# Optimization experiments

Measured on AMD Instinct MI355X. Metric: run time of the kernel, lower is better.

Reference implementation:

```python
import jax, jax.numpy as jnp
import numpy as np

B, T, F_DIM = 256, 96, 368
D_MODEL = min(768, F_DIM)   # d_model = min(hidden_dim, feat_dim)
NUM_CLASSES = 29
WINDOW = 5


def setup_inputs() -> dict:
    key = jax.random.key(0)
    ks = jax.random.split(key, 12)
    s_in = 1.0 / np.sqrt(F_DIM)
    s_h = 1.0 / np.sqrt(D_MODEL)
    return {
        "features": jax.random.normal(ks[0], (B, T, F_DIM), jnp.float32),
        "hand": jax.random.uniform(ks[1], (B, 2), jnp.float32),
        # single-layer GRU params (torch layout: (3H, in) / (3H, H))
        "gru_Wi": jax.random.normal(ks[2], (3 * D_MODEL, F_DIM), jnp.float32) * s_in,
        "gru_Wh": jax.random.normal(ks[3], (3 * D_MODEL, D_MODEL), jnp.float32) * s_h,
        "gru_bi": jax.random.normal(ks[4], (3 * D_MODEL,), jnp.float32) * s_h,
        "gru_bh": jax.random.normal(ks[5], (3 * D_MODEL,), jnp.float32) * s_h,
        # coarse predictor: Linear(d_model, 2)
        "Wc": jax.random.normal(ks[6], (2, D_MODEL), jnp.float32) * s_h,
        "bc": jax.random.normal(ks[7], (2,), jnp.float32) * s_h,
        # fine predictor: Linear(d_model, num_classes)
        "Wf": jax.random.normal(ks[8], (NUM_CLASSES, D_MODEL), jnp.float32) * s_h,
        "bf": jax.random.normal(ks[9], (NUM_CLASSES,), jnp.float32) * s_h,
    }


def _gru(x, Wi, Wh, bi, bh):
    """Single-layer unidirectional GRU (torch gate math). x: (B,T,F) -> (B,T,H)."""
    H = Wh.shape[1]
    xproj = jnp.einsum("btf,gf->btg", x, Wi) + bi  # (B,T,3H)

    def step(h, xt):
        gi_r, gi_z, gi_n = jnp.split(xt, 3, axis=-1)
        gh = h @ Wh.T + bh
        gh_r, gh_z, gh_n = jnp.split(gh, 3, axis=-1)
        r = jax.nn.sigmoid(gi_r + gh_r)
        z = jax.nn.sigmoid(gi_z + gh_z)
        n = jnp.tanh(gi_n + r * gh_n)
        h_new = (1.0 - z) * n + z * h
        return h_new, h_new

    h0 = jnp.zeros((x.shape[0], H), x.dtype)
    _, hs = jax.lax.scan(step, h0, jnp.swapaxes(xproj, 0, 1))  # (T,B,H)
    return jnp.swapaxes(hs, 0, 1)


def _apply_nms(scores):
    """Vectorized version of the per-position sliding-window min suppression.
    scores: (B,T,2). Keep row i iff scores[:, i, 0] equals the min of its
    window of size WINDOW (clipped at sequence boundaries)."""
    bg = scores[..., 0]  # (B,T)
    half = WINDOW // 2
    padded = jnp.pad(bg, ((0, 0), (half, half)), constant_values=jnp.inf)
    Tlen = bg.shape[1]
    shifts = jnp.stack([padded[:, k:k + Tlen] for k in range(WINDOW)], axis=0)
    wmin = jnp.min(shifts, axis=0)  # (B,T)
    keep = (bg == wmin)[..., None]
    return jnp.where(keep, scores, jnp.zeros_like(scores))


def reference(features, hand, gru_Wi, gru_Wh, gru_bi, gru_bh, Wc, bc, Wf, bf):
    # hand is accepted (matching the torch forward signature) but unused there too.
    temporal = _gru(features, gru_Wi, gru_Wh, gru_bi, gru_bh)  # (B,T,D)
    coarse_logits = temporal @ Wc.T + bc                        # (B,T,2)
    fine_logits = temporal @ Wf.T + bf                          # (B,T,C)
    coarse_scores = jax.nn.softmax(coarse_logits, axis=2)
    fine_scores = jax.nn.sigmoid(fine_logits)
    coarse_nms = _apply_nms(coarse_scores)
    coarse_decisions = jnp.argmax(coarse_nms, axis=2)
    return coarse_decisions, coarse_nms, fine_scores
```

## Files before the change

kernel.cpp:

```cpp
#include <hip/hip_runtime.h>
#include <hip/hip_bf16.h>

#define B_ 256
#define T_ 96
#define F_ 368
#define H_ 368
#define G3_ 1104
#define NC_ 29
#define BT_ (B_*T_)
#define HB_ (H_*B_)

#define NSL 8
#define NU 46
#define NCOL 138
#define ROWS 8
#define WQCOLS 1152

#define WQ2_U16 (8*9*12*2*64*8)

#define F4C(v, i) ((i)==0?(v).x:((i)==1?(v).y:((i)==2?(v).z:(v).w)))

typedef __attribute__((ext_vector_type(8))) short bhalf8;
typedef __attribute__((ext_vector_type(4))) float f32x4;

__device__ __forceinline__ unsigned short f2bf(float x) {
    unsigned u = __float_as_uint(x);
    u += 0x7fffu + ((u >> 16) & 1u);
    return (unsigned short)(u >> 16);
}
__device__ __forceinline__ float bf2f(unsigned short b) {
    return __uint_as_float(((unsigned)b) << 16);
}

__device__ __forceinline__ void gll16(const void* g, void* l) {
    __builtin_amdgcn_global_load_lds(
        (const __attribute__((address_space(1))) void*)g,
        (__attribute__((address_space(3))) void*)l, 16, 0, 0);
}

__device__ __forceinline__ int bload_i(const int* p) {
    return __hip_atomic_load(p, __ATOMIC_RELAXED, __HIP_MEMORY_SCOPE_AGENT);
}
__device__ __forceinline__ void bstore_i(int* p, int v) {
    __hip_atomic_store(p, v, __ATOMIC_RELAXED, __HIP_MEMORY_SCOPE_AGENT);
}
__device__ __forceinline__ unsigned int bload_u(const unsigned int* p) {
    return __hip_atomic_load(p, __ATOMIC_RELAXED, __HIP_MEMORY_SCOPE_AGENT);
}
__device__ __forceinline__ void bstore_u(unsigned int* p, unsigned int v) {
    __hip_atomic_store(p, v, __ATOMIC_RELAXED, __HIP_MEMORY_SCOPE_AGENT);
}

__global__ __launch_bounds__(256) void k_prep_wq2(const float* __restrict__ Wh,
                                                  unsigned short* __restrict__ Wq2) {
    const int idx = blockIdx.x*256 + threadIdx.x;
    const int l = idx & 63;
    const int p = (idx >> 6) & 1;
    int q = idx >> 7;
    const int kt = q % 12; q /= 12;
    const int nt = q % 9;
    const int us = q / 9;
    const int col = nt*16 + (l & 15);
    const int k0 = kt*32 + (l >> 4)*8;
    float v[8];
    #pragma unroll
    for (int e = 0; e < 8; ++e) v[e] = 0.f;
    if (col < NCOL && k0 < H_) {
        const int g = col / NU, uu = col - g*NU;
        const int grow = g*H_ + us*NU + uu;
        const float4 f0 = *reinterpret_cast<const float4*>(Wh + (size_t)grow*H_ + k0);
        const float4 f1 = *reinterpret_cast<const float4*>(Wh + (size_t)grow*H_ + k0 + 4);
        v[0]=f0.x; v[1]=f0.y; v[2]=f0.z; v[3]=f0.w;
        v[4]=f1.x; v[5]=f1.y; v[6]=f1.z; v[7]=f1.w;
    }
    unsigned int o[4];
    #pragma unroll
    for (int e = 0; e < 4; ++e) {
        const unsigned short h0 = f2bf(v[2*e]), h1 = f2bf(v[2*e+1]);
        const unsigned short w0 = p ? f2bf(v[2*e]   - bf2f(h0)) : h0;
        const unsigned short w1 = p ? f2bf(v[2*e+1] - bf2f(h1)) : h1;
        o[e] = (unsigned)w0 | ((unsigned)w1 << 16);
    }
    uint4* dst = reinterpret_cast<uint4*>(Wq2 + (size_t)idx*8);
    *dst = make_uint4(o[0], o[1], o[2], o[3]);
}

__global__ __launch_bounds__(256) void k_prep_wcat(const float* __restrict__ Wc,
                                                   const float* __restrict__ Wf,
                                                   float* __restrict__ Wcat) {
    const int idx = blockIdx.x*256 + threadIdx.x;
    const int u = idx >> 5, c = idx & 31;
    float v = 0.f;
    if (c < 2) v = Wc[c*H_ + u];
    else if (c < 31) v = Wf[(c-2)*H_ + u];
    Wcat[idx] = v;
}

__global__ __launch_bounds__(256) void k_zero_bar(int* __restrict__ bar) {
    __hip_atomic_store(bar + blockIdx.x*256 + threadIdx.x, 0,
                       __ATOMIC_RELAXED, __HIP_MEMORY_SCOPE_AGENT);
}

__global__ __launch_bounds__(256) void k_split_a(const float* __restrict__ src,
                                                 unsigned short* __restrict__ Ah,
                                                 unsigned short* __restrict__ Al) {
    const int idx = blockIdx.x*256 + threadIdx.x;
    const float4 v = reinterpret_cast<const float4*>(src)[idx];
    ushort4 h, lo;
    h.x = f2bf(v.x); lo.x = f2bf(v.x - bf2f(h.x));
    h.y = f2bf(v.y); lo.y = f2bf(v.y - bf2f(h.y));
    h.z = f2bf(v.z); lo.z = f2bf(v.z - bf2f(h.z));
    h.w = f2bf(v.w); lo.w = f2bf(v.w - bf2f(h.w));
    reinterpret_cast<ushort4*>(Ah)[idx] = h;
    reinterpret_cast<ushort4*>(Al)[idx] = lo;
}

__global__ __launch_bounds__(256) void k_split_b(const float* __restrict__ Wi,
                                                 unsigned short* __restrict__ Bh,
                                                 unsigned short* __restrict__ Bl) {
    const int idx = blockIdx.x*256 + threadIdx.x;
    const float x = (idx < G3_*F_) ? Wi[idx] : 0.f;
    const unsigned short h = f2bf(x);
    Bh[idx] = h;
    Bl[idx] = f2bf(x - bf2f(h));
}

__global__ __launch_bounds__(256) void k_xproj_mfma(
        const unsigned short* __restrict__ Ah, const unsigned short* __restrict__ Al,
        const unsigned short* __restrict__ Bh, const unsigned short* __restrict__ Bl,
        const float* __restrict__ bias, float* __restrict__ C)
{
    __shared__ unsigned short sAh[128*32], sAl[128*32], sBh[128*32], sBl[128*32];
    const int tid = threadIdx.x;
    const int w   = tid >> 6, l = tid & 63;
    const int gm0 = blockIdx.y * 128, gn0 = blockIdx.x * 128;

    const int srow = tid >> 2;
    const int cg   = (tid & 3) ^ ((tid >> 3) & 3);
    const size_t aoff0 = (size_t)(gm0 + srow)      * F_ + cg * 8;
    const size_t aoff1 = (size_t)(gm0 + srow + 64) * F_ + cg * 8;
    const size_t boff0 = (size_t)(gn0 + srow)      * F_ + cg * 8;
    const size_t boff1 = (size_t)(gn0 + srow + 64) * F_ + cg * 8;
    const int lb0 = w * 1024, lb1 = 4096 + w * 1024;

    const int lr = l & 15, lk = l >> 4;
    const int cswz = (lk ^ ((lr >> 1) & 3)) * 16;
    const int wr = w >> 1, wc = w & 1;
    int offA[4], offB[4];
    #pragma unroll
    for (int f = 0; f < 4; ++f) {
        offA[f] = (wr*64 + f*16 + lr) * 64 + cswz;
        offB[f] = (wc*64 + f*16 + lr) * 64 + cswz;
    }

    f32x4 acc[4][4];
    #pragma unroll
    for (int i = 0; i < 4; ++i)
        #pragma unroll
        for (int j = 0; j < 4; ++j) acc[i][j] = f32x4{0.f,0.f,0.f,0.f};

    auto stage = [&](int kt) {
        const size_t ko = (size_t)kt * 32;
        gll16(Ah + aoff0 + ko, (char*)sAh + lb0);
        gll16(Ah + aoff1 + ko, (char*)sAh + lb1);
        gll16(Al + aoff0 + ko, (char*)sAl + lb0);
        gll16(Al + aoff1 + ko, (char*)sAl + lb1);
        gll16(Bh + boff0 + ko, (char*)sBh + lb0);
        gll16(Bh + boff1 + ko, (char*)sBh + lb1);
        gll16(Bl + boff0 + ko, (char*)sBl + lb0);
        gll16(Bl + boff1 + ko, (char*)sBl + lb1);
    };

    stage(0);
    for (int kt = 0; kt < 12; ++kt) {
        __syncthreads();
        if (kt == 11) {
            if (cg >= 2) {
                const f32x4 z = f32x4{0.f,0.f,0.f,0.f};
                *reinterpret_cast<f32x4*>((char*)sAh + tid*16)        = z;
                *reinterpret_cast<f32x4*>((char*)sAh + tid*16 + 4096) = z;
                *reinterpret_cast<f32x4*>((char*)sAl + tid*16)        = z;
                *reinterpret_cast<f32x4*>((char*)sAl + tid*16 + 4096) = z;
                *reinterpret_cast<f32x4*>((char*)sBh + tid*16)        = z;
                *reinterpret_cast<f32x4*>((char*)sBh + tid*16 + 4096) = z;
                *reinterpret_cast<f32x4*>((char*)sBl + tid*16)        = z;
                *reinterpret_cast<f32x4*>((char*)sBl + tid*16 + 4096) = z;
            }
            __syncthreads();
        }
        bhalf8 fAh[4], fAl[4], fBh[4], fBl[4];
        #pragma unroll
        for (int f = 0; f < 4; ++f) {
            fAh[f] = *reinterpret_cast<const bhalf8*>((const char*)sAh + offA[f]);
            fAl[f] = *reinterpret_cast<const bhalf8*>((const char*)sAl + offA[f]);
            fBh[f] = *reinterpret_cast<const bhalf8*>((const char*)sBh + offB[f]);
            fBl[f] = *reinterpret_cast<const bhalf8*>((const char*)sBl + offB[f]);
        }
        __syncthreads();
        if (kt < 11) stage(kt + 1);
        #pragma unroll
        for (int i = 0; i < 4; ++i)
            #pragma unroll
            for (int j = 0; j < 4; ++j) {
                acc[i][j] = __builtin_amdgcn_mfma_f32_16x16x32_bf16(fAh[i], fBh[j], acc[i][j], 0, 0, 0);
                acc[i][j] = __builtin_amdgcn_mfma_f32_16x16x32_bf16(fAh[i], fBl[j], acc[i][j], 0, 0, 0);
                acc[i][j] = __builtin_amdgcn_mfma_f32_16x16x32_bf16(fAl[i], fBh[j], acc[i][j], 0, 0, 0);
            }
    }

    #pragma unroll
    for (int j = 0; j < 4; ++j) {
        const int gcol = gn0 + wc*64 + j*16 + lr;
        if (gcol < G3_) {
            const float bv = bias[gcol];
            #pragma unroll
            for (int i = 0; i < 4; ++i) {
                const int grow = gm0 + wr*64 + i*16 + lk*4;
                float* cp = C + (size_t)grow * G3_ + gcol;
                #pragma unroll
                for (int q = 0; q < 4; ++q)
                    cp[(size_t)q * G3_] = acc[i][j][q] + bv;
            }
        }
    }
}

__global__ __launch_bounds__(512, 2) void k_gru_all(const float* __restrict__ xproj,
                                                    const unsigned short* __restrict__ Wq2,
                                                    const float* __restrict__ bh,
                                                    unsigned int* __restrict__ h2,
                                                    int* __restrict__ bar) {
    __shared__ unsigned short sAh[48*16*8];
    __shared__ unsigned short sAl[48*16*8];
    __shared__ float part2[4][144][9];
    const int tid = threadIdx.x;
    const int us  = blockIdx.x & 7;
    const int bg  = blockIdx.x >> 3;
    const int b0  = bg * ROWS;
    const int w   = tid >> 6;
    const int l   = tid & 63;
    const int wk  = w >> 1;
    const int wn  = w & 1;
    const int nt0 = wn * 4;
    int* flags = bar + bg*64;
    int* myflag = flags + us;

    for (int s = tid; s < 48*16*8; s += 512) { sAh[s] = 0; sAl[s] = 0; }
    for (int s = tid; s < 4*144*9; s += 512) (&part2[0][0][0])[s] = 0.f;

    bhalf8 bB[5][3][2];
    #pragma unroll
    for (int ti = 0; ti < 5; ++ti)
        #pragma unroll
        for (int kti = 0; kti < 3; ++kti)
            #pragma unroll
            for (int p = 0; p < 2; ++p)
                bB[ti][kti][p] = *reinterpret_cast<const bhalf8*>(
                    Wq2 + ((((size_t)(us*9 + nt0 + ti)*12 + (wk*3 + kti))*2 + p)*64 + l)*8);

    const bool gact = tid < ROWS*NU;
    const int u1 = tid % NU, r1 = tid / NU;
    const int ug1 = us*NU + u1;
    float bh1r = 0.f, bh1z = 0.f, bh1n = 0.f;
    if (gact) { bh1r = bh[ug1]; bh1z = bh[H_+ug1]; bh1n = bh[2*H_+ug1]; }

    const int aoffb = (l >> 4)*256 + (l & 15)*16;

    __syncthreads();

    for (int t = 0; t < T_; ++t) {
        unsigned int* hout = h2 + (size_t)t*HB_;

        float xg10 = 0.f, xg11 = 0.f, xg12 = 0.f;
        if (gact) {
            const float* xr1 = xproj + ((size_t)(b0 + r1)*T_ + t)*G3_;
            xg10 = xr1[ug1]; xg11 = xr1[H_+ug1]; xg12 = xr1[2*H_+ug1];
        }

        if (t > 0) {
            while (bload_i(flags + w) < t) {}
            const unsigned int* hin = h2 + (size_t)(t - 1)*HB_;
            #pragma unroll
            for (int ii = 0; ii < 6; ++ii) {
                const int sl = l + ii*64;
                if (sl < NSL*NU) {
                    const int u = NU*w + (sl >> 3), r = sl & 7;
                    const unsigned int v = bload_u(hin + (size_t)u*B_ + b0 + r);
                    const int a = ((u >> 3)*16 + r)*8 + (u & 7);
                    sAh[a] = (unsigned short)(v & 0xffffu);
                    sAl[a] = (unsigned short)(v >> 16);
                }
            }
            __syncthreads();
            f32x4 acc[5];
            #pragma unroll
            for (int ti = 0; ti < 5; ++ti) acc[ti] = f32x4{0.f,0.f,0.f,0.f};
            #pragma unroll
            for (int kti = 0; kti < 3; ++kti) {
                const int kt = wk*3 + kti;
                const bhalf8 fh = *reinterpret_cast<const bhalf8*>((const char*)sAh + kt*1024 + aoffb);
                const bhalf8 fl = *reinterpret_cast<const bhalf8*>((const char*)sAl + kt*1024 + aoffb);
                #pragma unroll
                for (int ti = 0; ti < 5; ++ti) {
                    acc[ti] = __builtin_amdgcn_mfma_f32_16x16x32_bf16(fh, bB[ti][kti][0], acc[ti], 0, 0, 0);
                    acc[ti] = __builtin_amdgcn_mfma_f32_16x16x32_bf16(fh, bB[ti][kti][1], acc[ti], 0, 0, 0);
                    acc[ti] = __builtin_amdgcn_mfma_f32_16x16x32_bf16(fl, bB[ti][kti][0], acc[ti], 0, 0, 0);
                }
            }
            if (l < 32) {
                #pragma unroll
                for (int ti = 0; ti < 5; ++ti) {
                    const int col = (nt0 + ti)*16 + (l & 15);
                    float* pp = &part2[wk][col][(l >> 4)*4];
                    pp[0] = acc[ti][0]; pp[1] = acc[ti][1];
                    pp[2] = acc[ti][2]; pp[3] = acc[ti][3];
                }
            }
        }
        __syncthreads();

        if (gact) {
            float s0 = 0.f, s1 = 0.f, s2 = 0.f;
            #pragma unroll
            for (int q2 = 0; q2 < 4; ++q2) {
                s0 += part2[q2][u1][r1];
                s1 += part2[q2][NU + u1][r1];
                s2 += part2[q2][2*NU + u1][r1];
            }
            const float rg = 1.f/(1.f + expf(-(xg10 + s0 + bh1r)));
            const float zg = 1.f/(1.f + expf(-(xg11 + s1 + bh1z)));
            const float ng = tanhf(xg12 + rg*(s2 + bh1n));
            float hp = 0.f;
            if (t > 0) {
                const int a = ((ug1 >> 3)*16 + r1)*8 + (ug1 & 7);
                hp = bf2f(sAh[a]) + bf2f(sAl[a]);
            }
            const float hn = (1.f - zg)*ng + zg*hp;
            const unsigned short hi = f2bf(hn);
            const unsigned short lo = f2bf(hn - bf2f(hi));
            bstore_u(hout + (size_t)ug1*B_ + b0 + r1,
                     (unsigned)hi | ((unsigned)lo << 16));
        }
        __syncthreads();
        if (tid == 0) bstore_i(myflag, t + 1);
    }
}

__global__ __launch_bounds__(256) void k_heads2(const unsigned int* __restrict__ temporal2,
                                                const float* __restrict__ Wcat,
                                                const float* __restrict__ bc,
                                                const float* __restrict__ bf,
                                                float* __restrict__ cs,
                                                float* __restrict__ fine_out) {
    const int t = blockIdx.x;
    const int b = threadIdx.x;
    const unsigned int* tb = temporal2 + (size_t)t*HB_ + b;
    float acc[31];
    #pragma unroll
    for (int c = 0; c < 31; ++c) acc[c] = 0.f;
    for (int u = 0; u < H_; ++u) {
        const unsigned int v = tb[(size_t)u*B_];
        const float x = bf2f((unsigned short)(v & 0xffffu)) + bf2f((unsigned short)(v >> 16));
        const float* wrow = Wcat + u*32;
        #pragma unroll
        for (int c = 0; c < 31; ++c) acc[c] = fmaf(x, wrow[c], acc[c]);
    }
    const float l0 = acc[0] + bc[0], l1 = acc[1] + bc[1];
    const float m  = fmaxf(l0, l1);
    const float e0 = expf(l0 - m), e1 = expf(l1 - m);
    const float inv = 1.f/(e0 + e1);
    cs[((size_t)b*T_ + t)*2]     = e0*inv;
    cs[((size_t)b*T_ + t)*2 + 1] = e1*inv;
    #pragma unroll
    for (int c = 2; c < 31; ++c) {
        fine_out[((size_t)b*T_ + t)*NC_ + (c-2)] = 1.f/(1.f + expf(-(acc[c] + bf[c-2])));
    }
}

__global__ __launch_bounds__(256) void k_nms(const float* __restrict__ cs,
                                             float* __restrict__ out_dec,
                                             float* __restrict__ out_nms) {
    const int idx = blockIdx.x*256 + threadIdx.x;
    const int t = idx % T_;
    const float bg = cs[idx*2], s1 = cs[idx*2+1];
    float wmin = bg;
    #pragma unroll
    for (int dt = -2; dt <= 2; ++dt) {
        const int tt = t + dt;
        if (dt != 0 && tt >= 0 && tt < T_) wmin = fminf(wmin, cs[(idx + dt)*2]);
    }
    const bool keep = (bg <= wmin);
    out_dec[idx]     = (keep && (s1 > bg)) ? 1.f : 0.f;
    out_nms[idx*2]   = keep ? bg : 0.f;
    out_nms[idx*2+1] = keep ? s1 : 0.f;
}

extern "C" void kernel_launch(void* const* d_in, const int* in_sizes, int n_in,
                              void* d_out, int out_size, void* d_ws, size_t ws_size,
                              hipStream_t stream) {
    const float* features = (const float*)d_in[0];
    const float* Wi = (const float*)d_in[2];
    const float* Wh = (const float*)d_in[3];
    const float* bi = (const float*)d_in[4];
    const float* bh = (const float*)d_in[5];
    const float* Wc = (const float*)d_in[6];
    const float* bc = (const float*)d_in[7];
    const float* Wf = (const float*)d_in[8];
    const float* bf = (const float*)d_in[9];

    float* out = (float*)d_out;
    float* out_dec  = out;
    float* out_nms  = out + BT_;
    float* out_fine = out + BT_ + 2*BT_;

    float* xproj = (float*)d_ws;
    unsigned short* Wq2 = (unsigned short*)(xproj + (size_t)BT_*G3_);
    unsigned int* temporal2 = (unsigned int*)((char*)Wq2 + (size_t)WQ2_U16*2);
    int* bar = (int*)(temporal2 + (size_t)T_*HB_);
    float* Wcat = xproj;
    float* cs   = xproj + 12288;

    unsigned short* Bh16 = (unsigned short*)Wq2;
    unsigned short* Bl16 = Bh16 + (size_t)WQCOLS*F_;
    unsigned short* Ah16 = (unsigned short*)temporal2;
    unsigned short* Al16 = Ah16 + (size_t)BT_*F_;

    k_zero_bar<<<8, 256, 0, stream>>>(bar);
    k_split_a<<<8832, 256, 0, stream>>>(features, Ah16, Al16);
    k_split_b<<<1656, 256, 0, stream>>>(Wi, Bh16, Bl16);
    k_xproj_mfma<<<dim3(9, 192), 256, 0, stream>>>(Ah16, Al16, Bh16, Bl16, bi, xproj);
    k_prep_wq2<<<432, 256, 0, stream>>>(Wh, Wq2);
    k_gru_all<<<256, 512, 0, stream>>>(xproj, Wq2, bh, temporal2, bar);
    k_prep_wcat<<<46, 256, 0, stream>>>(Wc, Wf, Wcat);
    k_heads2<<<96, 256, 0, stream>>>(temporal2, Wcat, bc, bf, cs, out_fine);
    k_nms<<<96, 256, 0, stream>>>(cs, out_dec, out_nms);
}
```

Before: 730.7 us.

## Replace GRU flag barrier with sentinel-value polling on hidden-state data

Removes the per-step flag counters between cooperating blocks. The whole hidden-state buffer is pre-filled with a NaN sentinel, and consumers poll the data words directly until no lane sees the sentinel. This cuts one global round trip (flag write, then data read) per timestep, and a lighter LDS-only barrier replaces __syncthreads. In exchange it adds a full-buffer fill kernel of about 36 MB. It also relies on the per-word stores becoming visible without a release fence, and on the bf16 hi/lo pair never equalling the sentinel bit pattern.

```diff
diff --git a/kernel.cpp b/kernel.cpp
--- a/kernel.cpp
+++ b/kernel.cpp
@@ -18,6 +18,8 @@
 
 #define WQ2_U16 (8*9*12*2*64*8)
 
+#define SENT 0x7FC07FC0u
+
 #define F4C(v, i) ((i)==0?(v).x:((i)==1?(v).y:((i)==2?(v).z:(v).w)))
 
 typedef __attribute__((ext_vector_type(8))) short bhalf8;
@@ -38,17 +40,15 @@
         (__attribute__((address_space(3))) void*)l, 16, 0, 0);
 }
 
-__device__ __forceinline__ int bload_i(const int* p) {
-    return __hip_atomic_load(p, __ATOMIC_RELAXED, __HIP_MEMORY_SCOPE_AGENT);
-}
-__device__ __forceinline__ void bstore_i(int* p, int v) {
-    __hip_atomic_store(p, v, __ATOMIC_RELAXED, __HIP_MEMORY_SCOPE_AGENT);
-}
 __device__ __forceinline__ unsigned int bload_u(const unsigned int* p) {
     return __hip_atomic_load(p, __ATOMIC_RELAXED, __HIP_MEMORY_SCOPE_AGENT);
 }
 __device__ __forceinline__ void bstore_u(unsigned int* p, unsigned int v) {
     __hip_atomic_store(p, v, __ATOMIC_RELAXED, __HIP_MEMORY_SCOPE_AGENT);
+}
+
+__device__ __forceinline__ void barrier_lds() {
+    asm volatile("s_waitcnt lgkmcnt(0)\ns_barrier" ::: "memory");
 }
 
 __global__ __launch_bounds__(256) void k_prep_wq2(const float* __restrict__ Wh,
@@ -96,9 +96,9 @@
     Wcat[idx] = v;
 }
 
-__global__ __launch_bounds__(256) void k_zero_bar(int* __restrict__ bar) {
-    __hip_atomic_store(bar + blockIdx.x*256 + threadIdx.x, 0,
-                       __ATOMIC_RELAXED, __HIP_MEMORY_SCOPE_AGENT);
+__global__ __launch_bounds__(256) void k_fill_sent(unsigned int* __restrict__ p) {
+    const int idx = blockIdx.x*256 + threadIdx.x;
+    reinterpret_cast<uint4*>(p)[idx] = make_uint4(SENT, SENT, SENT, SENT);
 }
 
 __global__ __launch_bounds__(256) void k_split_a(const float* __restrict__ src,
@@ -228,8 +228,7 @@
 __global__ __launch_bounds__(512, 2) void k_gru_all(const float* __restrict__ xproj,
                                                     const unsigned short* __restrict__ Wq2,
                                                     const float* __restrict__ bh,
-                                                    unsigned int* __restrict__ h2,
-                                                    int* __restrict__ bar) {
+                                                    unsigned int* __restrict__ h2) {
     __shared__ unsigned short sAh[48*16*8];
     __shared__ unsigned short sAl[48*16*8];
     __shared__ float part2[4][144][9];
@@ -242,8 +241,6 @@
     const int wk  = w >> 1;
     const int wn  = w & 1;
     const int nt0 = wn * 4;
-    int* flags = bar + bg*64;
-    int* myflag = flags + us;
 
     for (int s = tid; s < 48*16*8; s += 512) { sAh[s] = 0; sAl[s] = 0; }
     for (int s = tid; s < 4*144*9; s += 512) (&part2[0][0][0])[s] = 0.f;
@@ -264,6 +261,17 @@
     float bh1r = 0.f, bh1z = 0.f, bh1n = 0.f;
     if (gact) { bh1r = bh[ug1]; bh1z = bh[H_+ug1]; bh1n = bh[2*H_+ug1]; }
 
+    int goff[6], aoff[6]; bool sact[6];
+    #pragma unroll
+    for (int ii = 0; ii < 6; ++ii) {
+        const int sl = l + ii*64;
+        sact[ii] = sl < NSL*NU;
+        const int u = NU*w + ((sl < NSL*NU) ? (sl >> 3) : 0);
+        const int r = sl & 7;
+        goff[ii] = u*B_ + b0 + r;
+        aoff[ii] = ((u >> 3)*16 + r)*8 + (u & 7);
+    }
+
     const int aoffb = (l >> 4)*256 + (l & 15)*16;
 
     __syncthreads();
@@ -278,20 +286,29 @@
         }
 
         if (t > 0) {
-            while (bload_i(flags + w) < t) {}
             const unsigned int* hin = h2 + (size_t)(t - 1)*HB_;
+            unsigned int v[6];
+            bool ok;
+            do {
+                unsigned bad = 0u;
+                #pragma unroll
+                for (int ii = 0; ii < 6; ++ii) {
+                    v[ii] = 0u;
+                    if (sact[ii]) {
+                        v[ii] = bload_u(hin + goff[ii]);
+                        bad |= (v[ii] == SENT) ? 1u : 0u;
+                    }
+                }
+                ok = !__any(bad != 0u);
+            } while (!ok);
             #pragma unroll
             for (int ii = 0; ii < 6; ++ii) {
-                const int sl = l + ii*64;
-                if (sl < NSL*NU) {
-                    const int u = NU*w + (sl >> 3), r = sl & 7;
-                    const unsigned int v = bload_u(hin + (size_t)u*B_ + b0 + r);
-                    const int a = ((u >> 3)*16 + r)*8 + (u & 7);
-                    sAh[a] = (unsigned short)(v & 0xffffu);
-                    sAl[a] = (unsigned short)(v >> 16);
+                if (sact[ii]) {
+                    sAh[aoff[ii]] = (unsigned short)(v[ii] & 0xffffu);
+                    sAl[aoff[ii]] = (unsigned short)(v[ii] >> 16);
                 }
             }
-            __syncthreads();
+            barrier_lds();
             f32x4 acc[5];
             #pragma unroll
             for (int ti = 0; ti < 5; ++ti) acc[ti] = f32x4{0.f,0.f,0.f,0.f};
@@ -317,7 +334,7 @@
                 }
             }
         }
-        __syncthreads();
+        barrier_lds();
 
         if (gact) {
             float s0 = 0.f, s1 = 0.f, s2 = 0.f;
@@ -341,8 +358,7 @@
             bstore_u(hout + (size_t)ug1*B_ + b0 + r1,
                      (unsigned)hi | ((unsigned)lo << 16));
         }
-        __syncthreads();
-        if (tid == 0) bstore_i(myflag, t + 1);
+        barrier_lds();
     }
 }
 
@@ -416,7 +432,6 @@
     float* xproj = (float*)d_ws;
     unsigned short* Wq2 = (unsigned short*)(xproj + (size_t)BT_*G3_);
     unsigned int* temporal2 = (unsigned int*)((char*)Wq2 + (size_t)WQ2_U16*2);
-    int* bar = (int*)(temporal2 + (size_t)T_*HB_);
     float* Wcat = xproj;
     float* cs   = xproj + 12288;
 
@@ -425,12 +440,12 @@
     unsigned short* Ah16 = (unsigned short*)temporal2;
     unsigned short* Al16 = Ah16 + (size_t)BT_*F_;
 
-    k_zero_bar<<<8, 256, 0, stream>>>(bar);
     k_split_a<<<8832, 256, 0, stream>>>(features, Ah16, Al16);
     k_split_b<<<1656, 256, 0, stream>>>(Wi, Bh16, Bl16);
     k_xproj_mfma<<<dim3(9, 192), 256, 0, stream>>>(Ah16, Al16, Bh16, Bl16, bi, xproj);
     k_prep_wq2<<<432, 256, 0, stream>>>(Wh, Wq2);
-    k_gru_all<<<256, 512, 0, stream>>>(xproj, Wq2, bh, temporal2, bar);
+    k_fill_sent<<<8832, 256, 0, stream>>>(temporal2);
+    k_gru_all<<<256, 512, 0, stream>>>(xproj, Wq2, bh, temporal2);
     k_prep_wcat<<<46, 256, 0, stream>>>(Wc, Wf, Wcat);
     k_heads2<<<96, 256, 0, stream>>>(temporal2, Wcat, bc, bf, cs, out_fine);
     k_nms<<<96, 256, 0, stream>>>(cs, out_dec, out_nms);
```

After: 800.1 us. +9.5%, slower.

## Use per-wave cache-line flags and 64-bit hidden-state loads in GRU recurrence

Applied to the files above, without the earlier changes.

The inter-block barrier moves from one flag per block to per-wave flags, each block on its own cache line. Each of the six writer waves signals right after its own stores drain, and each consumer wave polls only the six flags of the producer it needs, using a wave-wide any-vote. The hidden-state gather also loads pairs of batch rows as 64-bit atomics, which halves the number of global loads per step. The aim is to cut the serial latency of each of the 96 recurrent steps. The cost is a larger barrier area and more polling traffic, and correctness now depends on s_waitcnt ordering the stores before each wave's flag is set.

```diff
diff --git a/kernel.cpp b/kernel.cpp
--- a/kernel.cpp
+++ b/kernel.cpp
@@ -49,6 +49,9 @@
 }
 __device__ __forceinline__ void bstore_u(unsigned int* p, unsigned int v) {
     __hip_atomic_store(p, v, __ATOMIC_RELAXED, __HIP_MEMORY_SCOPE_AGENT);
+}
+__device__ __forceinline__ unsigned long long bload_u2(const unsigned long long* p) {
+    return __hip_atomic_load(p, __ATOMIC_RELAXED, __HIP_MEMORY_SCOPE_AGENT);
 }
 
 __global__ __launch_bounds__(256) void k_prep_wq2(const float* __restrict__ Wh,
@@ -242,8 +245,8 @@
     const int wk  = w >> 1;
     const int wn  = w & 1;
     const int nt0 = wn * 4;
-    int* flags = bar + bg*64;
-    int* myflag = flags + us;
+    int* myline = bar + (bg*8 + us)*32;
+    int* pline  = bar + (bg*8 + w)*32;
 
     for (int s = tid; s < 48*16*8; s += 512) { sAh[s] = 0; sAl[s] = 0; }
     for (int s = tid; s < 4*144*9; s += 512) (&part2[0][0][0])[s] = 0.f;
@@ -264,6 +267,17 @@
     float bh1r = 0.f, bh1z = 0.f, bh1n = 0.f;
     if (gact) { bh1r = bh[ug1]; bh1z = bh[H_+ug1]; bh1n = bh[2*H_+ug1]; }
 
+    int goff[3], aoff2[3]; bool sact[3];
+    #pragma unroll
+    for (int ii = 0; ii < 3; ++ii) {
+        const int pi = l + ii*64;
+        sact[ii] = pi < 184;
+        const int pc = sact[ii] ? pi : 0;
+        const int u = NU*w + (pc >> 2), r2 = pc & 3;
+        goff[ii]  = u*B_ + b0 + 2*r2;
+        aoff2[ii] = ((u >> 3)*16 + 2*r2)*8 + (u & 7);
+    }
+
     const int aoffb = (l >> 4)*256 + (l & 15)*16;
 
     __syncthreads();
@@ -278,17 +292,23 @@
         }
 
         if (t > 0) {
-            while (bload_i(flags + w) < t) {}
+            {
+                int f;
+                do { f = (l < 6) ? bload_i(pline + l) : t; } while (__any(f < t));
+            }
             const unsigned int* hin = h2 + (size_t)(t - 1)*HB_;
             #pragma unroll
-            for (int ii = 0; ii < 6; ++ii) {
-                const int sl = l + ii*64;
-                if (sl < NSL*NU) {
-                    const int u = NU*w + (sl >> 3), r = sl & 7;
-                    const unsigned int v = bload_u(hin + (size_t)u*B_ + b0 + r);
-                    const int a = ((u >> 3)*16 + r)*8 + (u & 7);
-                    sAh[a] = (unsigned short)(v & 0xffffu);
-                    sAl[a] = (unsigned short)(v >> 16);
+            for (int ii = 0; ii < 3; ++ii) {
+                if (sact[ii]) {
+                    const unsigned long long v = bload_u2(
+                        reinterpret_cast<const unsigned long long*>(hin + goff[ii]));
+                    const unsigned int v0 = (unsigned int)v;
+                    const unsigned int v1 = (unsigned int)(v >> 32);
+                    const int a = aoff2[ii];
+                    sAh[a]     = (unsigned short)(v0 & 0xffffu);
+                    sAl[a]     = (unsigned short)(v0 >> 16);
+                    sAh[a + 8] = (unsigned short)(v1 & 0xffffu);
+                    sAl[a + 8] = (unsigned short)(v1 >> 16);
                 }
             }
             __syncthreads();
@@ -341,8 +361,11 @@
             bstore_u(hout + (size_t)ug1*B_ + b0 + r1,
                      (unsigned)hi | ((unsigned)lo << 16));
         }
+        if (w < 6) {
+            asm volatile("s_waitcnt vmcnt(0)" ::: "memory");
+            if (l == 0) bstore_i(myline + w, t + 1);
+        }
         __syncthreads();
-        if (tid == 0) bstore_i(myflag, t + 1);
     }
 }
 
@@ -425,7 +448,7 @@
     unsigned short* Ah16 = (unsigned short*)temporal2;
     unsigned short* Al16 = Ah16 + (size_t)BT_*F_;
 
-    k_zero_bar<<<8, 256, 0, stream>>>(bar);
+    k_zero_bar<<<32, 256, 0, stream>>>(bar);
     k_split_a<<<8832, 256, 0, stream>>>(features, Ah16, Al16);
     k_split_b<<<1656, 256, 0, stream>>>(Wi, Bh16, Bl16);
     k_xproj_mfma<<<dim3(9, 192), 256, 0, stream>>>(Ah16, Al16, Bh16, Bl16, bi, xproj);
```

Result: faster. 685.9 us (-6.1%).
